# Optimization experiments

Measured on AMD Instinct MI355X. Metric: run time of the kernel, lower is better.

## Reference

```python
import jax, jax.numpy as jnp
import numpy as np

N_NODES = 4096
N_GRAPHS = 128
D_IN = 128
HEADS = 4
KEY_SIZE = 32  # == num_channels
D_OUT = 32 * D_IN  # num_channels * irreps.dim


def setup_inputs() -> dict:
    key = jax.random.key(0)
    ks = jax.random.split(key, 5)
    nodes = jax.random.normal(ks[0], (N_NODES, D_IN), dtype=jnp.float32)
    # 128 graphs of 32 nodes each, packed: sum(n_node) == N_NODES
    n_node = jnp.full((N_GRAPHS,), N_NODES // N_GRAPHS, dtype=jnp.int32)
    s_in = 1.0 / np.sqrt(D_IN)
    s_h = 1.0 / np.sqrt(HEADS * KEY_SIZE)
    Wq = jax.random.normal(ks[1], (D_IN, HEADS, KEY_SIZE), dtype=jnp.float32) * s_in
    Wk = jax.random.normal(ks[2], (D_IN, HEADS, KEY_SIZE), dtype=jnp.float32) * s_in
    Wv = jax.random.normal(ks[3], (D_IN, HEADS, KEY_SIZE), dtype=jnp.float32) * s_in
    Wo = jax.random.normal(ks[4], (HEADS * KEY_SIZE, D_OUT), dtype=jnp.float32) * s_h
    bq = jnp.zeros((HEADS, KEY_SIZE), dtype=jnp.float32)
    bk = jnp.zeros((HEADS, KEY_SIZE), dtype=jnp.float32)
    bv = jnp.zeros((HEADS, KEY_SIZE), dtype=jnp.float32)
    bo = jnp.zeros((D_OUT,), dtype=jnp.float32)
    return {"nodes": nodes, "n_node": n_node, "Wq": Wq, "bq": bq,
            "Wk": Wk, "bk": bk, "Wv": Wv, "bv": bv, "Wo": Wo, "bo": bo}


def reference(nodes, n_node, Wq, bq, Wk, bk, Wv, bv, Wo, bo):
    N = nodes.shape[0]
    G = n_node.shape[0]
    # segment id per packed node (get_segment_ids)
    seg = jnp.repeat(jnp.arange(G), n_node, total_repeat_length=N)
    # per-head projections: [N, H, K]
    q = jnp.einsum('nd,dhk->nhk', nodes, Wq) + bq
    k = jnp.einsum('nd,dhk->nhk', nodes, Wk) + bk
    v = jnp.einsum('nd,dhk->nhk', nodes, Wv) + bv
    # dense logits masked to block-diagonal per-graph blocks: [H, N, N]
    logits = jnp.einsum('nhk,mhk->hnm', q, k) / jnp.sqrt(jnp.float32(KEY_SIZE))
    mask = seg[:, None] == seg[None, :]  # [N, N]
    logits = jnp.where(mask[None, :, :], logits, jnp.float32(-1e30))
    attn = jax.nn.softmax(logits, axis=-1)
    out = jnp.einsum('hnm,mhk->nhk', attn, v).reshape(N, HEADS * KEY_SIZE)
    return out @ Wo + bo  # [N, num_channels * d_in]
```

## Files before the change

kernel.cpp:

```cpp
#include <hip/hip_runtime.h>
#include <hip/hip_bf16.h>


typedef __attribute__((ext_vector_type(4))) float f32x4;
typedef __attribute__((ext_vector_type(8))) short s16x8;
typedef __attribute__((ext_vector_type(4))) short s16x4;
typedef __attribute__((ext_vector_type(8))) __bf16 bf16x8;

static __device__ __forceinline__ short f2bf(float f) {
  union { float f; unsigned u; } v; v.f = f;
  unsigned r = v.u + 0x7fffu + ((v.u >> 16) & 1u);
  return (short)(r >> 16);
}

static __device__ __forceinline__ f32x4 mfma16(s16x8 a, s16x8 b, f32x4 c) {
  return __builtin_amdgcn_mfma_f32_16x16x32_bf16(
      __builtin_bit_cast(bf16x8, a), __builtin_bit_cast(bf16x8, b), c, 0, 0, 0);
}

__global__ __launch_bounds__(256) void k0_prep(
    const float* __restrict__ nodes,
    const float* __restrict__ Wq, const float* __restrict__ Wk,
    const float* __restrict__ Wv, const float* __restrict__ Wo,
    unsigned short* __restrict__ WqkvT, unsigned short* __restrict__ WoT,
    unsigned short* __restrict__ nodesBF)
{
  const int b = blockIdx.x;
  const int t = threadIdx.x;

  if (b >= 70) {
    const int r0 = (b - 70) << 6;
    const float* src = nodes + r0 * 128;
    unsigned short* dst = nodesBF + r0 * 128;
    #pragma unroll
    for (int i = 0; i < 8; ++i) {
      int idx = (i * 256 + t) << 2;
      float4 v = *(const float4*)(src + idx);
      s16x4 p;
      p[0] = f2bf(v.x); p[1] = f2bf(v.y); p[2] = f2bf(v.z); p[3] = f2bf(v.w);
      *(s16x4*)(dst + idx) = p;
    }
    return;
  }

  __shared__ alignas(16) short sT[64][136];
  const float* in; unsigned short* out; int C; int n0;
  if (b < 64)      { in = Wo; out = WoT;           C = 4096; n0 = b << 6; }
  else if (b < 66) { in = Wq; out = WqkvT;         C = 128;  n0 = (b - 64) << 6; }
  else if (b < 68) { in = Wk; out = WqkvT + 16384; C = 128;  n0 = (b - 66) << 6; }
  else             { in = Wv; out = WqkvT + 32768; C = 128;  n0 = (b - 68) << 6; }
  const int rr = t >> 4;
  const int c4 = (t & 15) << 2;
  #pragma unroll
  for (int i = 0; i < 8; ++i) {
    int r = i * 16 + rr;
    float4 v = *(const float4*)(in + r * C + n0 + c4);
    sT[c4 + 0][r] = f2bf(v.x);
    sT[c4 + 1][r] = f2bf(v.y);
    sT[c4 + 2][r] = f2bf(v.z);
    sT[c4 + 3][r] = f2bf(v.w);
  }
  __syncthreads();
  const int c  = t >> 2;
  const int k0 = (t & 3) << 5;
  #pragma unroll
  for (int j = 0; j < 4; ++j)
    *(s16x8*)&out[(n0 + c) * 128 + k0 + j * 8] = *(const s16x8*)&sT[c][k0 + j * 8];
}

__global__ __launch_bounds__(128) void k1_qkv_attn(
    const unsigned short* __restrict__ nodesBF,
    const unsigned short* __restrict__ WqkvT,
    const float* __restrict__ bq, const float* __restrict__ bk,
    const float* __restrict__ bv,
    unsigned short* __restrict__ attout)
{
  const int g = blockIdx.x;
  const int h = blockIdx.y;
  const int t = threadIdx.x;
  const int wv   = t >> 6;
  const int lane = t & 63;
  const int l15  = lane & 15;
  const int qd   = lane >> 4;
  const int mrow = wv << 4;

  __shared__ alignas(16) short sQ[32][40];
  __shared__ alignas(16) short sK[32][40];
  __shared__ alignas(16) short sVT[32][40];
  __shared__ alignas(16) short sP[32][40];

  s16x8 afrag[4];
  const unsigned short* nb = nodesBF + (g * 32 + mrow + l15) * 128 + qd * 8;
  #pragma unroll
  for (int kk = 0; kk < 4; ++kk) afrag[kk] = *(const s16x8*)(nb + kk * 32);

  s16x8 bfr[3][4][2];
  #pragma unroll
  for (int m3 = 0; m3 < 3; ++m3) {
    const unsigned short* WT = WqkvT + m3 * 16384 + (h * 32 + l15) * 128 + qd * 8;
    #pragma unroll
    for (int kk = 0; kk < 4; ++kk)
      #pragma unroll
      for (int nt = 0; nt < 2; ++nt)
        bfr[m3][kk][nt] = *(const s16x8*)(WT + nt * 16 * 128 + kk * 32);
  }
  const float* Bm[3] = {bq, bk, bv};

  #pragma unroll
  for (int m3 = 0; m3 < 3; ++m3) {
    f32x4 acc[2];
    f32x4 zero = {0.f, 0.f, 0.f, 0.f};
    acc[0] = zero; acc[1] = zero;
    #pragma unroll
    for (int kk = 0; kk < 4; ++kk)
      #pragma unroll
      for (int nt = 0; nt < 2; ++nt)
        acc[nt] = mfma16(afrag[kk], bfr[m3][kk][nt], acc[nt]);
    float b0 = Bm[m3][h * 32 + l15];
    float b1 = Bm[m3][h * 32 + 16 + l15];
    #pragma unroll
    for (int nt = 0; nt < 2; ++nt) {
      float bb = nt ? b1 : b0;
      #pragma unroll
      for (int r = 0; r < 4; ++r) {
        int m = mrow + qd * 4 + r;
        int c = nt * 16 + l15;
        float val = acc[nt][r] + bb;
        if (m3 == 0)      sQ[m][c]  = f2bf(val * 0.17677669529663687f);
        else if (m3 == 1) sK[m][c]  = f2bf(val);
        else              sVT[c][m] = f2bf(val);
      }
    }
  }
  __syncthreads();

  s16x8 qf = *(const s16x8*)&sQ[mrow + l15][qd * 8];
  s16x8 kf[2];
  #pragma unroll
  for (int nt = 0; nt < 2; ++nt) kf[nt] = *(const s16x8*)&sK[nt * 16 + l15][qd * 8];
  f32x4 sacc[2];
  {
    f32x4 zero = {0.f, 0.f, 0.f, 0.f};
    sacc[0] = mfma16(qf, kf[0], zero);
    sacc[1] = mfma16(qf, kf[1], zero);
  }

  #pragma unroll
  for (int r = 0; r < 4; ++r) {
    float a0 = sacc[0][r], a1 = sacc[1][r];
    float mx = fmaxf(a0, a1);
    mx = fmaxf(mx, __shfl_xor(mx, 1, 64));
    mx = fmaxf(mx, __shfl_xor(mx, 2, 64));
    mx = fmaxf(mx, __shfl_xor(mx, 4, 64));
    mx = fmaxf(mx, __shfl_xor(mx, 8, 64));
    float e0 = __expf(a0 - mx), e1 = __expf(a1 - mx);
    float s = e0 + e1;
    s += __shfl_xor(s, 1, 64);
    s += __shfl_xor(s, 2, 64);
    s += __shfl_xor(s, 4, 64);
    s += __shfl_xor(s, 8, 64);
    float inv = 1.0f / s;
    int m = mrow + qd * 4 + r;
    sP[m][l15]      = f2bf(e0 * inv);
    sP[m][16 + l15] = f2bf(e1 * inv);
  }

  s16x8 pf = *(const s16x8*)&sP[mrow + l15][qd * 8];
  s16x8 vf[2];
  #pragma unroll
  for (int nt = 0; nt < 2; ++nt) vf[nt] = *(const s16x8*)&sVT[nt * 16 + l15][qd * 8];
  f32x4 oacc[2];
  {
    f32x4 zero = {0.f, 0.f, 0.f, 0.f};
    oacc[0] = mfma16(pf, vf[0], zero);
    oacc[1] = mfma16(pf, vf[1], zero);
  }
  unsigned short* ao = attout + (g * 32 + mrow) * 128 + h * 32;
  #pragma unroll
  for (int nt = 0; nt < 2; ++nt)
    #pragma unroll
    for (int r = 0; r < 4; ++r)
      ao[(qd * 4 + r) * 128 + nt * 16 + l15] = (unsigned short)f2bf(oacc[nt][r]);
}

__global__ __launch_bounds__(256) void k3_gemm(
    const unsigned short* __restrict__ A,
    const unsigned short* __restrict__ BT,
    const float* __restrict__ bo,
    float* __restrict__ C)
{
  __shared__ alignas(16) short sA[128][136];
  __shared__ alignas(16) short sB[128][136];
  const int t  = threadIdx.x;
  const int m0 = blockIdx.y << 7;
  const int n0 = blockIdx.x << 7;

  #pragma unroll
  for (int i = 0; i < 8; ++i) {
    int id  = i * 256 + t;
    int row = id >> 4;
    int ch  = (id & 15) << 3;
    *(s16x8*)&sA[row][ch] = *(const s16x8*)(A  + (m0 + row) * 128 + ch);
    *(s16x8*)&sB[row][ch] = *(const s16x8*)(BT + (n0 + row) * 128 + ch);
  }
  __syncthreads();

  const int w    = t >> 6;
  const int lane = t & 63;
  const int l15  = lane & 15;
  const int qd   = lane >> 4;
  const int wm   = (w >> 1) << 6;
  const int wn   = (w & 1) << 6;

  f32x4 acc[4][4];
  {
    f32x4 zero = {0.f, 0.f, 0.f, 0.f};
    #pragma unroll
    for (int j = 0; j < 4; ++j)
      #pragma unroll
      for (int i = 0; i < 4; ++i) acc[j][i] = zero;
  }

  #pragma unroll
  for (int kk = 0; kk < 4; ++kk) {
    s16x8 af[4], bf[4];
    #pragma unroll
    for (int i = 0; i < 4; ++i)
      af[i] = *(const s16x8*)&sA[wm + i * 16 + l15][kk * 32 + qd * 8];
    #pragma unroll
    for (int j = 0; j < 4; ++j)
      bf[j] = *(const s16x8*)&sB[wn + j * 16 + l15][kk * 32 + qd * 8];
    #pragma unroll
    for (int j = 0; j < 4; ++j)
      #pragma unroll
      for (int i = 0; i < 4; ++i)
        acc[j][i] = mfma16(bf[j], af[i], acc[j][i]);
  }

  f32x4 bv4[4];
  #pragma unroll
  for (int j = 0; j < 4; ++j)
    bv4[j] = *(const f32x4*)&bo[n0 + wn + j * 16 + qd * 4];

  #pragma unroll
  for (int i = 0; i < 4; ++i) {
    float* crow = C + (m0 + wm + i * 16 + l15) * 4096 + n0 + wn + qd * 4;
    #pragma unroll
    for (int j = 0; j < 4; ++j) {
      f32x4 v = acc[j][i] + bv4[j];
      *(f32x4*)(crow + j * 16) = v;
    }
  }
}

extern "C" void kernel_launch(void* const* d_in, const int* in_sizes, int n_in,
                              void* d_out, int out_size, void* d_ws, size_t ws_size,
                              hipStream_t stream) {
  const float* nodes = (const float*)d_in[0];
  const float* Wq = (const float*)d_in[2];
  const float* bq = (const float*)d_in[3];
  const float* Wk = (const float*)d_in[4];
  const float* bk = (const float*)d_in[5];
  const float* Wv = (const float*)d_in[6];
  const float* bv = (const float*)d_in[7];
  const float* Wo = (const float*)d_in[8];
  const float* bo = (const float*)d_in[9];
  float* out = (float*)d_out;

  unsigned short* attout  = (unsigned short*)d_ws;
  unsigned short* WoT     = attout + 4096 * 128;
  unsigned short* WqkvT   = WoT + 4096 * 128;
  unsigned short* nodesBF = WqkvT + 3 * 128 * 128;

  k0_prep<<<134, 256, 0, stream>>>(nodes, Wq, Wk, Wv, Wo, WqkvT, WoT, nodesBF);
  k1_qkv_attn<<<dim3(128, 4), 128, 0, stream>>>(nodesBF, WqkvT, bq, bk, bv, attout);
  k3_gemm<<<dim3(32, 32), 256, 0, stream>>>(attout, WoT, bo, out);
}
```

Baseline: 112.0 us.

## Fold bf16 conversion and weight transposes into consumer kernels, drop prep kernel

```diff
diff --git a/kernel.cpp b/kernel.cpp
--- a/kernel.cpp
+++ b/kernel.cpp
@@ -18,59 +18,10 @@
       __builtin_bit_cast(bf16x8, a), __builtin_bit_cast(bf16x8, b), c, 0, 0, 0);
 }
 
-__global__ __launch_bounds__(256) void k0_prep(
+__global__ __launch_bounds__(128) void k1_qkv_attn(
     const float* __restrict__ nodes,
     const float* __restrict__ Wq, const float* __restrict__ Wk,
-    const float* __restrict__ Wv, const float* __restrict__ Wo,
-    unsigned short* __restrict__ WqkvT, unsigned short* __restrict__ WoT,
-    unsigned short* __restrict__ nodesBF)
-{
-  const int b = blockIdx.x;
-  const int t = threadIdx.x;
-
-  if (b >= 70) {
-    const int r0 = (b - 70) << 6;
-    const float* src = nodes + r0 * 128;
-    unsigned short* dst = nodesBF + r0 * 128;
-    #pragma unroll
-    for (int i = 0; i < 8; ++i) {
-      int idx = (i * 256 + t) << 2;
-      float4 v = *(const float4*)(src + idx);
-      s16x4 p;
-      p[0] = f2bf(v.x); p[1] = f2bf(v.y); p[2] = f2bf(v.z); p[3] = f2bf(v.w);
-      *(s16x4*)(dst + idx) = p;
-    }
-    return;
-  }
-
-  __shared__ alignas(16) short sT[64][136];
-  const float* in; unsigned short* out; int C; int n0;
-  if (b < 64)      { in = Wo; out = WoT;           C = 4096; n0 = b << 6; }
-  else if (b < 66) { in = Wq; out = WqkvT;         C = 128;  n0 = (b - 64) << 6; }
-  else if (b < 68) { in = Wk; out = WqkvT + 16384; C = 128;  n0 = (b - 66) << 6; }
-  else             { in = Wv; out = WqkvT + 32768; C = 128;  n0 = (b - 68) << 6; }
-  const int rr = t >> 4;
-  const int c4 = (t & 15) << 2;
-  #pragma unroll
-  for (int i = 0; i < 8; ++i) {
-    int r = i * 16 + rr;
-    float4 v = *(const float4*)(in + r * C + n0 + c4);
-    sT[c4 + 0][r] = f2bf(v.x);
-    sT[c4 + 1][r] = f2bf(v.y);
-    sT[c4 + 2][r] = f2bf(v.z);
-    sT[c4 + 3][r] = f2bf(v.w);
-  }
-  __syncthreads();
-  const int c  = t >> 2;
-  const int k0 = (t & 3) << 5;
-  #pragma unroll
-  for (int j = 0; j < 4; ++j)
-    *(s16x8*)&out[(n0 + c) * 128 + k0 + j * 8] = *(const s16x8*)&sT[c][k0 + j * 8];
-}
-
-__global__ __launch_bounds__(128) void k1_qkv_attn(
-    const unsigned short* __restrict__ nodesBF,
-    const unsigned short* __restrict__ WqkvT,
+    const float* __restrict__ Wv,
     const float* __restrict__ bq, const float* __restrict__ bk,
     const float* __restrict__ bv,
     unsigned short* __restrict__ attout)
@@ -84,26 +35,48 @@
   const int qd   = lane >> 4;
   const int mrow = wv << 4;
 
+  __shared__ alignas(16) short sN[32][136];
+  __shared__ alignas(16) short sW[3][32][136];
   __shared__ alignas(16) short sQ[32][40];
   __shared__ alignas(16) short sK[32][40];
   __shared__ alignas(16) short sVT[32][40];
   __shared__ alignas(16) short sP[32][40];
 
+  const float* ng = nodes + g * 32 * 128;
+  #pragma unroll
+  for (int i = 0; i < 8; ++i) {
+    int f4  = i * 128 + t;
+    int row = f4 >> 5;
+    int c4  = (f4 & 31) << 2;
+    float4 v = *(const float4*)(ng + row * 128 + c4);
+    s16x4 p;
+    p[0] = f2bf(v.x); p[1] = f2bf(v.y); p[2] = f2bf(v.z); p[3] = f2bf(v.w);
+    *(s16x4*)&sN[row][c4] = p;
+  }
+
+  const float* Wm[3] = {Wq, Wk, Wv};
+  #pragma unroll
+  for (int m3 = 0; m3 < 3; ++m3) {
+    const float* src = Wm[m3];
+    #pragma unroll
+    for (int i = 0; i < 8; ++i) {
+      int c_idx = i * 128 + t;
+      int d   = c_idx >> 3;
+      int off = (c_idx & 7) << 2;
+      float4 v = *(const float4*)(src + d * 128 + h * 32 + off);
+      sW[m3][off + 0][d] = f2bf(v.x);
+      sW[m3][off + 1][d] = f2bf(v.y);
+      sW[m3][off + 2][d] = f2bf(v.z);
+      sW[m3][off + 3][d] = f2bf(v.w);
+    }
+  }
+  __syncthreads();
+
   s16x8 afrag[4];
-  const unsigned short* nb = nodesBF + (g * 32 + mrow + l15) * 128 + qd * 8;
-  #pragma unroll
-  for (int kk = 0; kk < 4; ++kk) afrag[kk] = *(const s16x8*)(nb + kk * 32);
-
-  s16x8 bfr[3][4][2];
-  #pragma unroll
-  for (int m3 = 0; m3 < 3; ++m3) {
-    const unsigned short* WT = WqkvT + m3 * 16384 + (h * 32 + l15) * 128 + qd * 8;
-    #pragma unroll
-    for (int kk = 0; kk < 4; ++kk)
-      #pragma unroll
-      for (int nt = 0; nt < 2; ++nt)
-        bfr[m3][kk][nt] = *(const s16x8*)(WT + nt * 16 * 128 + kk * 32);
-  }
+  #pragma unroll
+  for (int kk = 0; kk < 4; ++kk)
+    afrag[kk] = *(const s16x8*)&sN[mrow + l15][kk * 32 + qd * 8];
+
   const float* Bm[3] = {bq, bk, bv};
 
   #pragma unroll
@@ -114,8 +87,10 @@
     #pragma unroll
     for (int kk = 0; kk < 4; ++kk)
       #pragma unroll
-      for (int nt = 0; nt < 2; ++nt)
-        acc[nt] = mfma16(afrag[kk], bfr[m3][kk][nt], acc[nt]);
+      for (int nt = 0; nt < 2; ++nt) {
+        s16x8 bf = *(const s16x8*)&sW[m3][nt * 16 + l15][kk * 32 + qd * 8];
+        acc[nt] = mfma16(afrag[kk], bf, acc[nt]);
+      }
     float b0 = Bm[m3][h * 32 + l15];
     float b1 = Bm[m3][h * 32 + 16 + l15];
     #pragma unroll
@@ -185,7 +160,7 @@
 
 __global__ __launch_bounds__(256) void k3_gemm(
     const unsigned short* __restrict__ A,
-    const unsigned short* __restrict__ BT,
+    const float* __restrict__ Wo,
     const float* __restrict__ bo,
     float* __restrict__ C)
 {
@@ -200,8 +175,18 @@
     int id  = i * 256 + t;
     int row = id >> 4;
     int ch  = (id & 15) << 3;
-    *(s16x8*)&sA[row][ch] = *(const s16x8*)(A  + (m0 + row) * 128 + ch);
-    *(s16x8*)&sB[row][ch] = *(const s16x8*)(BT + (n0 + row) * 128 + ch);
+    *(s16x8*)&sA[row][ch] = *(const s16x8*)(A + (m0 + row) * 128 + ch);
+  }
+  #pragma unroll
+  for (int i = 0; i < 16; ++i) {
+    int id   = i * 256 + t;
+    int k    = id >> 5;
+    int noff = (id & 31) << 2;
+    float4 v = *(const float4*)(Wo + k * 4096 + n0 + noff);
+    sB[noff + 0][k] = f2bf(v.x);
+    sB[noff + 1][k] = f2bf(v.y);
+    sB[noff + 2][k] = f2bf(v.z);
+    sB[noff + 3][k] = f2bf(v.w);
   }
   __syncthreads();
 
@@ -267,12 +252,9 @@
   const float* bo = (const float*)d_in[9];
   float* out = (float*)d_out;
 
-  unsigned short* attout  = (unsigned short*)d_ws;
-  unsigned short* WoT     = attout + 4096 * 128;
-  unsigned short* WqkvT   = WoT + 4096 * 128;
-  unsigned short* nodesBF = WqkvT + 3 * 128 * 128;
-
-  k0_prep<<<134, 256, 0, stream>>>(nodes, Wq, Wk, Wv, Wo, WqkvT, WoT, nodesBF);
-  k1_qkv_attn<<<dim3(128, 4), 128, 0, stream>>>(nodesBF, WqkvT, bq, bk, bv, attout);
-  k3_gemm<<<dim3(32, 32), 256, 0, stream>>>(attout, WoT, bo, out);
-}
+  unsigned short* attout = (unsigned short*)d_ws;
+
+  k1_qkv_attn<<<dim3(128, 4), 128, 0, stream>>>(nodes, Wq, Wk, Wv,
+                                                bq, bk, bv, attout);
+  k3_gemm<<<dim3(32, 32), 256, 0, stream>>>(attout, Wo, bo, out);
+}
```

Result: slower. 117.6 us (+5.0%).
